# Kernel optimization log

Hardware: AMD Instinct MI355X
Metric: run time of the kernel (lower is better)

Reference implementation:

```python
import jax, jax.numpy as jnp
import numpy as np

E = 512   # embed_size
H = 8     # num_heads
D = E // H
N = 4
T = 2048


def quantize(x, b, e):
    # fake-quant: scale by 2^e, clamp to signed b-bit range, floor, dequant
    s = jnp.exp2(e)
    lo = -jnp.exp2(b - 1.0)
    hi = jnp.exp2(b - 1.0) - 1.0
    return jnp.floor(jnp.clip(x / s, lo, hi)) * s


def setup_inputs() -> dict:
    key = jax.random.key(0)
    ks = jax.random.split(key, 8)
    f = lambda k, shape: jax.random.normal(k, shape, dtype=jnp.float32)
    w = 1.0 / np.sqrt(E)  # ~ torch Linear init scale
    return {
        "values": f(ks[0], (N, T, E)),
        "keys": f(ks[1], (N, T, E)),
        "query": f(ks[2], (N, T, E)),
        "Wq": f(ks[3], (E, E)) * w, "bq": jnp.zeros((E,), jnp.float32),
        "Wk": f(ks[4], (E, E)) * w, "bk": jnp.zeros((E,), jnp.float32),
        "Wv": f(ks[5], (E, E)) * w, "bv": jnp.zeros((E,), jnp.float32),
        "Wo": f(ks[6], (E, E)) * w, "bo": jnp.zeros((E,), jnp.float32),
        "b_param": jnp.float32(8.0),
        "e_param": jnp.float32(0.0),
    }


def reference(values, keys, query, Wq, bq, Wk, bk, Wv, bv, Wo, bo, b_param, e_param):
    n, t, emb = query.shape
    d = emb // H
    # linear projections (torch Linear: x @ W^T + b), split heads -> [N,H,T,D]
    q = (query @ Wq.T + bq).reshape(n, t, H, d).transpose(0, 2, 1, 3)
    k = (keys @ Wk.T + bk).reshape(n, t, H, d).transpose(0, 2, 1, 3)
    v = (values @ Wv.T + bv).reshape(n, t, H, d).transpose(0, 2, 1, 3)
    b = jnp.clip(b_param, 1.0, 8.0)
    q = quantize(q, b, e_param)
    k = quantize(k, b, e_param)
    v = quantize(v, b, e_param)
    # NOTE: source scales by sqrt(embed_size), not sqrt(head_dim)
    energy = jnp.einsum('nhqd,nhkd->nhqk', q, k) / jnp.sqrt(jnp.float32(emb))
    attn = jax.nn.softmax(energy, axis=-1)
    out = jnp.einsum('nhqk,nhkd->nhqd', attn, v)
    out = out.transpose(0, 2, 1, 3).reshape(n, t, emb)
    return out @ Wo.T + bo
```

## Files before the change

### kernel.cpp

```cpp
#include <hip/hip_runtime.h>
#include <hip/hip_bf16.h>
#include <hip/hip_fp16.h>
#include <cstdint>
#include <cstddef>


typedef __attribute__((ext_vector_type(8))) _Float16 f16x8;
typedef __attribute__((ext_vector_type(2))) __fp16 hf16x2;
typedef __attribute__((ext_vector_type(16))) float f32x16;
typedef __attribute__((ext_vector_type(4))) unsigned u32x4;
typedef unsigned short u16;

#define EL  4194304
#define WEL 262144

static __device__ __forceinline__ u16 f2h(float x) {
  _Float16 h = (_Float16)x;
  return __builtin_bit_cast(u16, h);
}
static __device__ __forceinline__ unsigned pkh2(float a, float b) {
  hf16x2 p = __builtin_amdgcn_cvt_pkrtz(a, b);
  return __builtin_bit_cast(unsigned, p);
}
static __device__ __forceinline__ void gl_lds16(const void* g, void* l) {
  __builtin_amdgcn_global_load_lds(
      (__attribute__((address_space(1))) void*)g,
      (__attribute__((address_space(3))) void*)l, 16, 0, 0);
}

struct PrepAllArgs { const float* src[7]; };

__global__ __launch_bounds__(256) void prep_all_kernel(PrepAllArgs a,
                                                       u16* __restrict__ dst)
{
  const int i = blockIdx.x * 256 + threadIdx.x;
  const float* src; int off;
  if (i < 3145728) {
    const int m = i >> 20; off = i & 1048575;
    src = (m == 0) ? a.src[0] : (m == 1) ? a.src[1] : a.src[2];
  } else {
    const int j = i - 3145728; const int w = j >> 16; off = j & 65535;
    src = (w == 0) ? a.src[3] : (w == 1) ? a.src[4]
        : (w == 2) ? a.src[5] : a.src[6];
  }
  const float4 v = ((const float4*)src)[off];
  ushort4 o;
  o.x = f2h(v.x); o.y = f2h(v.y); o.z = f2h(v.z); o.w = f2h(v.w);
  ((ushort4*)dst)[i] = o;
}

struct ProjArgs {
  const u16* X[3]; const u16* W[3]; const float* bias[3];
  u16* dst[3]; int trans[3];
};

__global__ __launch_bounds__(256, 3) void proj_kernel(ProjArgs args,
    const float* __restrict__ bparam, const float* __restrict__ eparam)
{
  __shared__ u16 sm[17408];
  u16* const As = sm;
  u16* const Bs = sm + 8192;

  const int z = blockIdx.z;
  const u16* __restrict__ X = args.X[z];
  const u16* __restrict__ W = args.W[z];
  const float* __restrict__ bias = args.bias[z];
  u16* __restrict__ dst = args.dst[z];
  const int mode = args.trans[z];

  const int tid  = threadIdx.x;
  const int lane = tid & 63;
  const int wave = tid >> 6;
  const int lam  = lane & 31;
  const int hl   = lane >> 5;
  const int wm   = wave & 1;
  const int wn   = wave >> 1;
  const int mbase = blockIdx.x * 128;
  const int nbase = blockIdx.y * 128;

  const int srow = tid >> 3;
  const int sj   = (tid & 7) ^ (srow & 7);
  const u16* gA = X + (size_t)(mbase + srow) * 512 + sj * 8;
  const u16* gB = W + (size_t)(nbase + srow) * 512 + sj * 8;

  int offA[2][4], offB[2][4];
#pragma unroll
  for (int f = 0; f < 2; ++f)
#pragma unroll
    for (int kk = 0; kk < 4; ++kk) {
      const int c = 2 * kk + hl;
      const int m = wm * 64 + f * 32 + lam;
      offA[f][kk] = m * 128 + ((c ^ (m & 7)) * 16);
      const int nn = wn * 64 + f * 32 + lam;
      offB[f][kk] = nn * 128 + ((c ^ (nn & 7)) * 16);
    }

  f32x16 acc[2][2];
#pragma unroll
  for (int a = 0; a < 2; ++a)
#pragma unroll
    for (int b = 0; b < 2; ++b)
#pragma unroll
      for (int i = 0; i < 16; ++i) acc[a][b][i] = 0.f;

  for (int kt = 0; kt < 512; kt += 64) {
    __syncthreads();
#pragma unroll
    for (int t = 0; t < 4; ++t) {
      gl_lds16(gA + kt + t * 32 * 512, (char*)As + tid * 16 + t * 4096);
      gl_lds16(gB + kt + t * 32 * 512, (char*)Bs + tid * 16 + t * 4096);
    }
    __syncthreads();

    f16x8 fA[2][4], fB[2][4];
#pragma unroll
    for (int f = 0; f < 2; ++f)
#pragma unroll
      for (int kk = 0; kk < 4; ++kk) {
        fA[f][kk] = *(const f16x8*)((const char*)As + offA[f][kk]);
        fB[f][kk] = *(const f16x8*)((const char*)Bs + offB[f][kk]);
      }
#pragma unroll
    for (int mf = 0; mf < 2; ++mf)
#pragma unroll
      for (int nf = 0; nf < 2; ++nf)
#pragma unroll
        for (int kk = 0; kk < 4; ++kk)
          acc[mf][nf] = __builtin_amdgcn_mfma_f32_32x32x16_f16(
              fA[mf][kk], fB[nf][kk], acc[mf][nf], 0, 0, 0);
  }

  const float bq   = fminf(fmaxf(bparam[0], 1.0f), 8.0f);
  const float e    = eparam[0];
  const float s    = exp2f(e);
  const float invs = exp2f(-e);
  const float qlo  = -exp2f(bq - 1.0f);
  const float qhi  = exp2f(bq - 1.0f) - 1.0f;
  const int nidx = mbase >> 11;
  const int tb   = mbase & 2047;
  const int hb   = nbase >> 6;

  if (mode == 0) {
#pragma unroll
    for (int mf = 0; mf < 2; ++mf)
#pragma unroll
      for (int nf = 0; nf < 2; ++nf)
#pragma unroll
        for (int reg = 0; reg < 16; ++reg) {
          int col = wn * 64 + nf * 32 + lam;
          int row = wm * 64 + mf * 32 + (reg & 3) + 8 * (reg >> 2) + 4 * hl;
          float v = acc[mf][nf][reg] + bias[nbase + col];
          float qv = floorf(fminf(fmaxf(v * invs, qlo), qhi)) * s;
          dst[((size_t)(nidx * 8 + hb + (col >> 6)) * 2048 + tb + row) * 64 +
              (col & 63)] = f2h(qv);
        }
  } else if (mode == 1) {
#pragma unroll
    for (int mf = 0; mf < 2; ++mf)
#pragma unroll
      for (int nf = 0; nf < 2; ++nf)
#pragma unroll
        for (int reg = 0; reg < 16; ++reg) {
          int col = wn * 64 + nf * 32 + lam;
          int row = wm * 64 + mf * 32 + (reg & 3) + 8 * (reg >> 2) + 4 * hl;
          float v = acc[mf][nf][reg] + bias[nbase + col];
          float qv = floorf(fminf(fmaxf(v * invs, qlo), qhi)) * s;
          const int t = tb + row;
          const int d = col & 63;
          dst[(size_t)(nidx * 8 + hb + (col >> 6)) * 131072 +
              (t >> 5) * 2048 + (t & 31) * 64 + (((d >> 3) ^ (t & 7)) << 3) +
              (d & 7)] = f2h(qv);
        }
  } else {
    __syncthreads();
#pragma unroll
    for (int mf = 0; mf < 2; ++mf)
#pragma unroll
      for (int nf = 0; nf < 2; ++nf)
#pragma unroll
        for (int reg = 0; reg < 16; ++reg) {
          int col = wn * 64 + nf * 32 + lam;
          int row = wm * 64 + mf * 32 + (reg & 3) + 8 * (reg >> 2) + 4 * hl;
          float v = acc[mf][nf][reg] + bias[nbase + col];
          float qv = floorf(fminf(fmaxf(v * invs, qlo), qhi)) * s;
          sm[col * 136 + row] = f2h(qv);
        }
    __syncthreads();
    const int r = tid >> 1, half = tid & 1;
    const u16* sp = sm + r * 136 + half * 64;
    const int d  = r & 63;
    const int sb = d & 1;
    const int rx = (d >> 1) & 7;
    u16* const gp0 = dst + (size_t)(nidx * 8 + hb + (r >> 6)) * 131072 +
                     (d >> 1) * 64;
#pragma unroll
    for (int i = 0; i < 8; ++i) {
      const int t = tb + half * 64 + i * 8;
      const int c = (t & 31) >> 3;
      const int s2 = ((c << 1) | sb) ^ rx;
      *(uint4*)(gp0 + (t >> 5) * 2048 + s2 * 8) = *(const uint4*)(sp + i * 8);
    }
  }
}

__global__ __launch_bounds__(256, 2) void attn_kernel(
    const u16* __restrict__ qbuf, const u16* __restrict__ kbuf,
    const u16* __restrict__ vtbuf, u16* __restrict__ ctx)
{
  __shared__ u16 sm[17920];
  char* const smc = (char*)sm;

  const int tid  = threadIdx.x;
  const int wave = tid >> 6;
  const int lane = tid & 63;
  const int lam  = lane & 31;
  const int hl   = lane >> 5;
  const int bid = blockIdx.x;
  const int wg  = (bid & 7) * 128 + (bid >> 3);
  const int qt = wg & 31;
  const int nh = wg >> 5;
  const int hd = nh & 7;
  const int n  = nh >> 3;
  const int qbase = qt * 64;

  const u16* Qp = qbuf + ((size_t)nh * 2048 + qbase) * 64;
  const u16* gK = kbuf  + (size_t)nh * 131072 + wave * 2048 + lane * 8;
  const u16* gV = vtbuf + (size_t)nh * 131072 + wave * 2048 + lane * 8;
  char* const kvb = smc + wave * 8192;

  f16x8 qf[2][4];
#pragma unroll
  for (int qb = 0; qb < 2; ++qb)
#pragma unroll
    for (int dk = 0; dk < 4; ++dk)
      qf[qb][dk] = *(const f16x8*)(Qp + (qb * 32 + lam) * 64 + dk * 16 + hl * 8);
#pragma unroll
  for (int qb = 0; qb < 2; ++qb)
#pragma unroll
    for (int dk = 0; dk < 4; ++dk)
      asm volatile("" :: "v"(qf[qb][dk]));

  auto stage4 = [&](const u16* src, char* dstb) {
#pragma unroll
    for (int r = 0; r < 4; ++r)
      gl_lds16(src + r * 512, dstb + r * 1024 + lane * 16);
  };

  stage4(gK, kvb);
  stage4(gV, kvb + 4096);

  int offK[4];
#pragma unroll
  for (int dk = 0; dk < 4; ++dk)
    offK[dk] = lam * 128 + (((2 * dk + hl) ^ (lam & 7)) << 4);
  int offV[2][2];
#pragma unroll
  for (int nf = 0; nf < 2; ++nf)
#pragma unroll
    for (int kkl = 0; kkl < 2; ++kkl) {
      const int R = nf * 16 + (lam >> 1);
      const int s2 = (((2 * kkl + hl) << 1) | (lam & 1)) ^ (R & 7);
      offV[nf][kkl] = 4096 + R * 128 + s2 * 16;
    }

  const float sc = (float)(1.4426950408889634 / 22.627416997969522);

  float l_acc[2] = {0.f, 0.f};
  f32x16 O[2][2];
#pragma unroll
  for (int a = 0; a < 2; ++a)
#pragma unroll
    for (int b = 0; b < 2; ++b)
#pragma unroll
      for (int i = 0; i < 16; ++i) O[a][b][i] = 0.f;

  for (int t = 0; t < 16; ++t) {
    asm volatile("s_waitcnt vmcnt(4)" ::: "memory");
    f16x8 Kf[4];
#pragma unroll
    for (int dk = 0; dk < 4; ++dk)
      Kf[dk] = *(const f16x8*)(kvb + offK[dk]);
    asm volatile("s_waitcnt lgkmcnt(0)" ::: "memory");
    stage4(gK + ((t + 1) & 15) * 8192, kvb);

    f16x8 pfrag[2][2];
#pragma unroll
    for (int qb = 0; qb < 2; ++qb) {
      f32x16 S;
#pragma unroll
      for (int i = 0; i < 16; ++i) S[i] = 0.f;
      __builtin_amdgcn_s_setprio(1);
#pragma unroll
      for (int dk = 0; dk < 4; ++dk)
        S = __builtin_amdgcn_mfma_f32_32x32x16_f16(Kf[dk], qf[qb][dk],
                                                   S, 0, 0, 0);
      __builtin_amdgcn_s_setprio(0);
      unsigned pk[4][2];
#pragma unroll
      for (int gh = 0; gh < 4; ++gh) {
        float p0 = __builtin_amdgcn_exp2f(S[4 * gh + 0] * sc);
        float p1 = __builtin_amdgcn_exp2f(S[4 * gh + 1] * sc);
        float p2 = __builtin_amdgcn_exp2f(S[4 * gh + 2] * sc);
        float p3 = __builtin_amdgcn_exp2f(S[4 * gh + 3] * sc);
        l_acc[qb] += (p0 + p1) + (p2 + p3);
        pk[gh][0] = pkh2(p0, p1);
        pk[gh][1] = pkh2(p2, p3);
      }
#pragma unroll
      for (int kkl = 0; kkl < 2; ++kkl) {
        unsigned s0 = hl ? pk[2 * kkl][0] : pk[2 * kkl + 1][0];
        unsigned s1 = hl ? pk[2 * kkl][1] : pk[2 * kkl + 1][1];
        unsigned o0 = hl ? pk[2 * kkl + 1][0] : pk[2 * kkl][0];
        unsigned o1 = hl ? pk[2 * kkl + 1][1] : pk[2 * kkl][1];
        unsigned rr0 = (unsigned)__shfl_xor((int)s0, 32);
        unsigned rr1 = (unsigned)__shfl_xor((int)s1, 32);
        u32x4 f;
        f[0] = hl ? rr0 : o0;
        f[1] = hl ? rr1 : o1;
        f[2] = hl ? o0 : rr0;
        f[3] = hl ? o1 : rr1;
        pfrag[qb][kkl] = __builtin_bit_cast(f16x8, f);
      }
    }

    asm volatile("s_waitcnt vmcnt(4)" ::: "memory");
    f16x8 Vf[2][2];
#pragma unroll
    for (int nf = 0; nf < 2; ++nf)
#pragma unroll
      for (int kkl = 0; kkl < 2; ++kkl)
        Vf[nf][kkl] = *(const f16x8*)(kvb + offV[nf][kkl]);
    asm volatile("s_waitcnt lgkmcnt(0)" ::: "memory");
    stage4(gV + ((t + 1) & 15) * 8192, kvb + 4096);

    __builtin_amdgcn_s_setprio(1);
#pragma unroll
    for (int qb = 0; qb < 2; ++qb)
#pragma unroll
      for (int nf = 0; nf < 2; ++nf)
#pragma unroll
        for (int kkl = 0; kkl < 2; ++kkl)
          O[qb][nf] = __builtin_amdgcn_mfma_f32_32x32x16_f16(
              pfrag[qb][kkl], Vf[nf][kkl], O[qb][nf], 0, 0, 0);
    __builtin_amdgcn_s_setprio(0);
  }

  asm volatile("s_waitcnt vmcnt(0)" ::: "memory");
#pragma unroll
  for (int qb = 0; qb < 2; ++qb) l_acc[qb] += __shfl_xor(l_acc[qb], 32);
  float* lred = (float*)(smc + 34816);
  if (hl == 0) {
    lred[wave * 64 + lam]      = l_acc[0];
    lred[wave * 64 + 32 + lam] = l_acc[1];
  }
  __syncthreads();

  const int q  = tid >> 3;
  const int dc = (tid & 7) * 8;
#pragma unroll
  for (int qb = 0; qb < 2; ++qb) {
    float* Ow = (float*)(smc + wave * 8704);
#pragma unroll
    for (int nf = 0; nf < 2; ++nf)
#pragma unroll
      for (int r = 0; r < 16; ++r) {
        const int qrow = (r & 3) + 8 * (r >> 2) + 4 * hl;
        Ow[qrow * 68 + nf * 32 + lam] = O[qb][nf][r];
      }
    __syncthreads();
    float a[8];
    {
      const char* b = smc + q * 272 + dc * 4;
      const float4 v0 = *(const float4*)b;
      const float4 v1 = *(const float4*)(b + 16);
      a[0] = v0.x; a[1] = v0.y; a[2] = v0.z; a[3] = v0.w;
      a[4] = v1.x; a[5] = v1.y; a[6] = v1.z; a[7] = v1.w;
    }
#pragma unroll
    for (int w = 1; w < 4; ++w) {
      const char* b = smc + w * 8704 + q * 272 + dc * 4;
      const float4 v0 = *(const float4*)b;
      const float4 v1 = *(const float4*)(b + 16);
      a[0] += v0.x; a[1] += v0.y; a[2] += v0.z; a[3] += v0.w;
      a[4] += v1.x; a[5] += v1.y; a[6] += v1.z; a[7] += v1.w;
    }
    const float lsum = lred[qb * 32 + q] + lred[64 + qb * 32 + q] +
                       lred[128 + qb * 32 + q] + lred[192 + qb * 32 + q];
    const float rinv = 1.0f / lsum;
    unsigned outp[4];
#pragma unroll
    for (int i = 0; i < 4; ++i)
      outp[i] = pkh2(a[2 * i] * rinv, a[2 * i + 1] * rinv);
    u16* cp = ctx + ((size_t)n * 2048 + qbase + qb * 32 + q) * 512 +
              hd * 64 + dc;
    *(uint4*)cp = *(const uint4*)outp;
    if (qb == 0) __syncthreads();
  }
}

__global__ __launch_bounds__(256) void outproj_kernel(
    const u16* __restrict__ ctxb, const u16* __restrict__ Wof,
    const float* __restrict__ bias, float* __restrict__ out)
{
  __shared__ u16 sm[12288];
  u16* const As = sm;
  u16* const Bs = sm + 4096;

  const int tid  = threadIdx.x;
  const int lane = tid & 63;
  const int wave = tid >> 6;
  const int lam  = lane & 31;
  const int hl   = lane >> 5;
  const int wm   = wave & 1;
  const int wn   = wave >> 1;
  const int mbase = blockIdx.x * 64;
  const int nbase = blockIdx.y * 128;

  const int srow = tid >> 3;
  const int sj   = (tid & 7) ^ (srow & 7);
  const u16* gA = ctxb + (size_t)(mbase + srow) * 512 + sj * 8;
  const u16* gB = Wof  + (size_t)(nbase + srow) * 512 + sj * 8;

  int offA[4], offB[2][4];
#pragma unroll
  for (int kk = 0; kk < 4; ++kk) {
    const int c = 2 * kk + hl;
    const int m = wm * 32 + lam;
    offA[kk] = m * 128 + ((c ^ (m & 7)) * 16);
#pragma unroll
    for (int f = 0; f < 2; ++f) {
      const int nn = wn * 64 + f * 32 + lam;
      offB[f][kk] = nn * 128 + ((c ^ (nn & 7)) * 16);
    }
  }

  f32x16 acc[2];
#pragma unroll
  for (int a = 0; a < 2; ++a)
#pragma unroll
    for (int i = 0; i < 16; ++i) acc[a][i] = 0.f;

  for (int kt = 0; kt < 512; kt += 64) {
    __syncthreads();
#pragma unroll
    for (int t = 0; t < 2; ++t)
      gl_lds16(gA + kt + t * 32 * 512, (char*)As + tid * 16 + t * 4096);
#pragma unroll
    for (int t = 0; t < 4; ++t)
      gl_lds16(gB + kt + t * 32 * 512, (char*)Bs + tid * 16 + t * 4096);
    __syncthreads();

    f16x8 fA[4], fB[2][4];
#pragma unroll
    for (int kk = 0; kk < 4; ++kk) {
      fA[kk] = *(const f16x8*)((const char*)As + offA[kk]);
#pragma unroll
      for (int f = 0; f < 2; ++f)
        fB[f][kk] = *(const f16x8*)((const char*)Bs + offB[f][kk]);
    }
#pragma unroll
    for (int nf = 0; nf < 2; ++nf)
#pragma unroll
      for (int kk = 0; kk < 4; ++kk)
        acc[nf] = __builtin_amdgcn_mfma_f32_32x32x16_f16(
            fA[kk], fB[nf][kk], acc[nf], 0, 0, 0);
  }

#pragma unroll
  for (int nf = 0; nf < 2; ++nf)
#pragma unroll
    for (int reg = 0; reg < 16; ++reg) {
      int col = nbase + wn * 64 + nf * 32 + lam;
      int row = mbase + wm * 32 + (reg & 3) + 8 * (reg >> 2) + 4 * hl;
      out[(size_t)row * 512 + col] = acc[nf][reg] + bias[col];
    }
}

extern "C" void kernel_launch(void* const* d_in, const int* in_sizes, int n_in,
                              void* d_out, int out_size, void* d_ws, size_t ws_size,
                              hipStream_t stream) {
  (void)in_sizes; (void)n_in; (void)out_size; (void)ws_size;
  const float* values = (const float*)d_in[0];
  const float* keys   = (const float*)d_in[1];
  const float* query  = (const float*)d_in[2];
  const float* Wq = (const float*)d_in[3];  const float* bq = (const float*)d_in[4];
  const float* Wk = (const float*)d_in[5];  const float* bk = (const float*)d_in[6];
  const float* Wv = (const float*)d_in[7];  const float* bv = (const float*)d_in[8];
  const float* Wo = (const float*)d_in[9];  const float* bo = (const float*)d_in[10];
  const float* bp = (const float*)d_in[11]; const float* ep = (const float*)d_in[12];

  u16* ws    = (u16*)d_ws;
  u16* qbuf  = ws;
  u16* kbuf  = ws + (size_t)EL;
  u16* vtbuf = ws + (size_t)2 * EL;
  u16* ctx   = ws + (size_t)3 * EL;
  u16* xwf   = ws + (size_t)4 * EL;

  PrepAllArgs pa;
  pa.src[0] = query; pa.src[1] = keys; pa.src[2] = values;
  pa.src[3] = Wq; pa.src[4] = Wk; pa.src[5] = Wv; pa.src[6] = Wo;
  prep_all_kernel<<<13312, 256, 0, stream>>>(pa, xwf);

  const float* Bsrc[3] = {bq, bk, bv};
  u16* Dst[3] = {qbuf, kbuf, vtbuf};
  ProjArgs a;
  for (int m = 0; m < 3; ++m) {
    a.X[m] = xwf + (size_t)m * EL;
    a.W[m] = xwf + (size_t)3 * EL + (size_t)m * WEL;
    a.bias[m] = Bsrc[m]; a.dst[m] = Dst[m]; a.trans[m] = m;
  }
  proj_kernel<<<dim3(64, 4, 3), 256, 0, stream>>>(a, bp, ep);

  attn_kernel<<<dim3(1024), 256, 0, stream>>>(qbuf, kbuf, vtbuf, ctx);
  outproj_kernel<<<dim3(128, 4), 256, 0, stream>>>(
      ctx, xwf + (size_t)3 * EL + (size_t)3 * WEL, bo, (float*)d_out);
}
```

Baseline: 189.5 us.

## Fold softmax scale into Q and permute V layout to drop P shuffles

The Q projection epilogue now multiplies the quantized values by log2(e)/sqrt(E) before storing, so the attention loop no longer scales each score before exp2. The transposed V store is reordered so that the key ordering of the stored V matches the register order of the exponentiated score fragments. This removes the cross-half-wave shuffles and selects that built the P operand. Pre-scaling Q changes fp16 rounding of Q slightly, and correctness now depends on the V layout permutation exactly matching the MFMA output ordering.

Result: no change. 186.3 us (-1.7%).

```diff
diff --git a/kernel.cpp b/kernel.cpp
--- a/kernel.cpp
+++ b/kernel.cpp
@@ -141,6 +141,7 @@
   const int hb   = nbase >> 6;
 
   if (mode == 0) {
+    const float SCQ = (float)(1.4426950408889634 / 22.627416997969522);
 #pragma unroll
     for (int mf = 0; mf < 2; ++mf)
 #pragma unroll
@@ -152,7 +153,7 @@
           float v = acc[mf][nf][reg] + bias[nbase + col];
           float qv = floorf(fminf(fmaxf(v * invs, qlo), qhi)) * s;
           dst[((size_t)(nidx * 8 + hb + (col >> 6)) * 2048 + tb + row) * 64 +
-              (col & 63)] = f2h(qv);
+              (col & 63)] = f2h(qv * SCQ);
         }
   } else if (mode == 1) {
 #pragma unroll
@@ -194,11 +195,17 @@
     u16* const gp0 = dst + (size_t)(nidx * 8 + hb + (r >> 6)) * 131072 +
                      (d >> 1) * 64;
 #pragma unroll
-    for (int i = 0; i < 8; ++i) {
-      const int t = tb + half * 64 + i * 8;
-      const int c = (t & 31) >> 3;
-      const int s2 = ((c << 1) | sb) ^ rx;
-      *(uint4*)(gp0 + (t >> 5) * 2048 + s2 * 8) = *(const uint4*)(sp + i * 8);
+    for (int kb = 0; kb < 2; ++kb) {
+      const int Bg = ((tb + half * 64) >> 5) + kb;
+#pragma unroll
+      for (int g = 0; g < 4; ++g) {
+        const int qoff = (g & 1) * 4 + (g >> 1) * 16;
+        const uint2 lo = *(const uint2*)(sp + kb * 32 + qoff);
+        const uint2 hi = *(const uint2*)(sp + kb * 32 + qoff + 8);
+        uint4 val; val.x = lo.x; val.y = lo.y; val.z = hi.x; val.w = hi.y;
+        const int s2 = ((g << 1) | sb) ^ rx;
+        *(uint4*)(gp0 + Bg * 2048 + s2 * 8) = val;
+      }
     }
   }
 }
@@ -263,8 +270,6 @@
       offV[nf][kkl] = 4096 + R * 128 + s2 * 16;
     }
 
-  const float sc = (float)(1.4426950408889634 / 22.627416997969522);
-
   float l_acc[2] = {0.f, 0.f};
   f32x16 O[2][2];
 #pragma unroll
@@ -295,32 +300,19 @@
         S = __builtin_amdgcn_mfma_f32_32x32x16_f16(Kf[dk], qf[qb][dk],
                                                    S, 0, 0, 0);
       __builtin_amdgcn_s_setprio(0);
-      unsigned pk[4][2];
+      u32x4 fr[2];
 #pragma unroll
       for (int gh = 0; gh < 4; ++gh) {
-        float p0 = __builtin_amdgcn_exp2f(S[4 * gh + 0] * sc);
-        float p1 = __builtin_amdgcn_exp2f(S[4 * gh + 1] * sc);
-        float p2 = __builtin_amdgcn_exp2f(S[4 * gh + 2] * sc);
-        float p3 = __builtin_amdgcn_exp2f(S[4 * gh + 3] * sc);
+        float p0 = __builtin_amdgcn_exp2f(S[4 * gh + 0]);
+        float p1 = __builtin_amdgcn_exp2f(S[4 * gh + 1]);
+        float p2 = __builtin_amdgcn_exp2f(S[4 * gh + 2]);
+        float p3 = __builtin_amdgcn_exp2f(S[4 * gh + 3]);
         l_acc[qb] += (p0 + p1) + (p2 + p3);
-        pk[gh][0] = pkh2(p0, p1);
-        pk[gh][1] = pkh2(p2, p3);
+        fr[gh >> 1][(gh & 1) * 2 + 0] = pkh2(p0, p1);
+        fr[gh >> 1][(gh & 1) * 2 + 1] = pkh2(p2, p3);
       }
-#pragma unroll
-      for (int kkl = 0; kkl < 2; ++kkl) {
-        unsigned s0 = hl ? pk[2 * kkl][0] : pk[2 * kkl + 1][0];
-        unsigned s1 = hl ? pk[2 * kkl][1] : pk[2 * kkl + 1][1];
-        unsigned o0 = hl ? pk[2 * kkl + 1][0] : pk[2 * kkl][0];
-        unsigned o1 = hl ? pk[2 * kkl + 1][1] : pk[2 * kkl][1];
-        unsigned rr0 = (unsigned)__shfl_xor((int)s0, 32);
-        unsigned rr1 = (unsigned)__shfl_xor((int)s1, 32);
-        u32x4 f;
-        f[0] = hl ? rr0 : o0;
-        f[1] = hl ? rr1 : o1;
-        f[2] = hl ? o0 : rr0;
-        f[3] = hl ? o1 : rr1;
-        pfrag[qb][kkl] = __builtin_bit_cast(f16x8, f);
-      }
+      pfrag[qb][0] = __builtin_bit_cast(f16x8, fr[0]);
+      pfrag[qb][1] = __builtin_bit_cast(f16x8, fr[1]);
     }
 
     asm volatile("s_waitcnt vmcnt(4)" ::: "memory");
```
